# Optimization experiments

Measured on AMD Instinct MI355X. Metric: run time of the kernel, lower is better.

The kernel has to match this reference:

```python
import jax, jax.numpy as jnp
import numpy as np
import math

B, S, H = 4, 2048, 1024
EMBED_DIM = 1024


def setup_inputs() -> dict:
    key = jax.random.key(0)
    ks = jax.random.split(key, 7)
    scale = 1.0 / math.sqrt(H)
    return {
        "xs": jax.random.normal(ks[0], (B, S, H), dtype=jnp.float32),
        "WQ_w": jax.random.normal(ks[1], (EMBED_DIM, H), dtype=jnp.float32) * scale,
        "WQ_b": jax.random.normal(ks[2], (EMBED_DIM,), dtype=jnp.float32) * scale,
        "WK_w": jax.random.normal(ks[3], (EMBED_DIM, H), dtype=jnp.float32) * scale,
        "WK_b": jax.random.normal(ks[4], (EMBED_DIM,), dtype=jnp.float32) * scale,
        "WV_w": jax.random.normal(ks[5], (EMBED_DIM, H), dtype=jnp.float32) * scale,
        "WV_b": jax.random.normal(ks[6], (EMBED_DIM,), dtype=jnp.float32) * scale,
    }


def reference(xs, WQ_w, WQ_b, WK_w, WK_b, WV_w, WV_b):
    # Linear projections (torch nn.Linear: x @ W.T + b)
    q = jnp.einsum('bsh,eh->bse', xs, WQ_w) + WQ_b  # [B,S,E]
    k = jnp.einsum('bsh,eh->bse', xs, WK_w) + WK_b
    v = jnp.einsum('bsh,eh->bse', xs, WV_w) + WV_b
    seq_len = xs.shape[1]
    inv_sqrt_e = 1.0 / math.sqrt(EMBED_DIM)
    qk = jnp.einsum('bqe,bke->bqk', q, k) * inv_sqrt_e  # [B,S,S]
    # causal mask: positions k > q get -inf (triu, diagonal=1)
    causal = jnp.tril(jnp.ones((seq_len, seq_len), dtype=bool))
    qk = jnp.where(causal[None, :, :], qk, -jnp.inf)
    attn = jax.nn.softmax(qk, axis=2)
    y = jnp.einsum('bqk,bke->bqe', attn, v)  # [B,S,E]
    return y
```

## Files before the change

### kernel.cpp

```cpp
#include <hip/hip_runtime.h>
#include <cstdint>
#include <cstddef>

typedef _Float16 f16;
typedef __attribute__((ext_vector_type(4))) _Float16 f16x4;
typedef __attribute__((ext_vector_type(8))) _Float16 f16x8;
typedef __attribute__((ext_vector_type(4))) float f32x4;

static constexpr int BB = 4;
static constexpr int SS = 2048;
static constexpr int EE = 1024;

static constexpr int BM = 128, BN = 128;

__device__ __forceinline__ void gload_lds16(const f16* g, f16* l) {
  __builtin_amdgcn_global_load_lds(
      (const __attribute__((address_space(1))) void*)g,
      (__attribute__((address_space(3))) void*)l, 16, 0, 0);
}

struct Frag {
  int lane, wave, wy, wx, l16, quad, quadx;
  __device__ Frag() {
    const int tid = threadIdx.x;
    lane = tid & 63; wave = tid >> 6;
    wy = wave >> 1; wx = wave & 1;
    l16 = lane & 15; quad = lane >> 4;
    quadx = quad ^ ((l16 >> 2) & 3);
  }
};

struct Stager {
  const f16* g[2];
  int l[2];
  __device__ void init(const f16* base, int ld, const Frag& fr) {
#pragma unroll
    for (int i = 0; i < 2; ++i) {
      const int c = fr.wave * 128 + i * 64 + fr.lane;
      const int row = c >> 2;
      const int kcs = (c & 3) ^ ((c >> 4) & 3);
      g[i] = base + (size_t)row * ld + kcs * 8;
      l[i] = c * 8;
    }
  }
  __device__ __forceinline__ void stage(int ko, f16* lds) const {
    gload_lds16(g[0] + ko, lds + l[0]);
    gload_lds16(g[1] + ko, lds + l[1]);
  }
};

__device__ __forceinline__ void mfma_round(
    const f16* __restrict__ Ash, const f16* __restrict__ Bsh,
    f32x4 acc[4][4], const Frag& fr)
{
  f16x8 af[4], bf[4];
#pragma unroll
  for (int mi = 0; mi < 4; ++mi)
    af[mi] = *(const f16x8*)(Ash + (fr.wy * 64 + mi * 16 + fr.l16) * 32 + fr.quadx * 8);
#pragma unroll
  for (int ni = 0; ni < 4; ++ni)
    bf[ni] = *(const f16x8*)(Bsh + (fr.wx * 64 + ni * 16 + fr.l16) * 32 + fr.quadx * 8);
#pragma unroll
  for (int mi = 0; mi < 4; ++mi)
#pragma unroll
    for (int ni = 0; ni < 4; ++ni)
      acc[mi][ni] = __builtin_amdgcn_mfma_f32_16x16x32_f16(af[mi], bf[ni], acc[mi][ni], 0, 0, 0);
}

__device__ __forceinline__ void gemm_core(
    const f16* __restrict__ A, const f16* __restrict__ Bt,
    int lda, int ldb, int kOuter,
    f16* __restrict__ Ash, f16* __restrict__ Bsh,
    f32x4 acc[4][4], const Frag& fr)
{
  Stager sa, sb;
  sa.init(A, lda, fr);
  sb.init(Bt, ldb, fr);
  for (int kt = 0; kt < kOuter; ++kt) {
    const int ko = kt * 64;
    sa.stage(ko, Ash);       sa.stage(ko + 32, Ash + 128 * 32);
    sb.stage(ko, Bsh);       sb.stage(ko + 32, Bsh + 128 * 32);
    __syncthreads();
    mfma_round(Ash, Bsh, acc, fr);
    mfma_round(Ash + 128 * 32, Bsh + 128 * 32, acc, fr);
    __syncthreads();
  }
}

__device__ __forceinline__ void gemm_core2(
    const f16* __restrict__ A, const f16* __restrict__ Bt,
    int lda, int ldb, int kOuter,
    f16* __restrict__ Ash, f16* __restrict__ Bsh,
    f32x4 acc[4][4], const Frag& fr)
{
  Stager sa, sb;
  sa.init(A, lda, fr);
  sb.init(Bt, ldb, fr);
  sa.stage(0, Ash);  sa.stage(32, Ash + 4096);
  sb.stage(0, Bsh);  sb.stage(32, Bsh + 4096);
  for (int kt = 0; kt < kOuter; ++kt) {
    const int cur = kt & 1, nxt = cur ^ 1;
    if (kt + 1 < kOuter) {
      const int ko = (kt + 1) * 64;
      sa.stage(ko, Ash + nxt * 8192);  sa.stage(ko + 32, Ash + nxt * 8192 + 4096);
      sb.stage(ko, Bsh + nxt * 8192);  sb.stage(ko + 32, Bsh + nxt * 8192 + 4096);
      asm volatile("s_waitcnt vmcnt(8)" ::: "memory");
    } else {
      asm volatile("s_waitcnt vmcnt(0)" ::: "memory");
    }
    __builtin_amdgcn_s_barrier();
    mfma_round(Ash + cur * 8192,        Bsh + cur * 8192,        acc, fr);
    mfma_round(Ash + cur * 8192 + 4096, Bsh + cur * 8192 + 4096, acc, fr);
    __builtin_amdgcn_s_barrier();
  }
}

__global__ __launch_bounds__(256) void cast_all_kernel(
    const float* __restrict__ xs,
    const float* __restrict__ w0, const float* __restrict__ w1, const float* __restrict__ w2,
    f16* __restrict__ Xh, f16* __restrict__ o0, f16* __restrict__ o1, f16* __restrict__ o2)
{
  const int i = blockIdx.x * 256 + threadIdx.x;
  const float* src; f16* dst; int idx;
  if (i < 2097152) {
    src = xs; dst = Xh; idx = i;
  } else {
    const int j = i - 2097152;
    const int w = j >> 18;
    idx = j & 262143;
    src = (w == 0) ? w0 : (w == 1) ? w1 : w2;
    dst = (w == 0) ? o0 : (w == 1) ? o1 : o2;
  }
  const float4 f = ((const float4*)src)[idx];
  f16x4 h;
  h.x = (f16)f.x; h.y = (f16)f.y; h.z = (f16)f.z; h.w = (f16)f.w;
  ((f16x4*)dst)[idx] = h;
}

__global__ __launch_bounds__(256, 2) void proj_kernel(
    const f16* __restrict__ X,
    const f16* __restrict__ Wq, const f16* __restrict__ Wk, const f16* __restrict__ Wv,
    const float* __restrict__ bq, const float* __restrict__ bk, const float* __restrict__ bv,
    f16* __restrict__ Qh, f16* __restrict__ Kh, f16* __restrict__ Vt)
{
  __shared__ __align__(16) f16 smem[3][2][BM * 32];
  Frag fr;
  const int t = blockIdx.x;
  if (t < 512) {
    const int row0 = (t & 63) * BM, col0 = (t >> 6) * BN;
    Stager sa, sw0, sw1;
    sa.init(X + (size_t)row0 * EE, EE, fr);
    sw0.init(Wq + (size_t)col0 * EE, EE, fr);
    sw1.init(Wk + (size_t)col0 * EE, EE, fr);

    f32x4 acc[2][4][4] = {};

    for (int kt = 0; kt < EE / 64; ++kt) {
      const int ko = kt * 64;
      sa.stage(ko, smem[0][0]);   sa.stage(ko + 32, smem[0][1]);
      sw0.stage(ko, smem[1][0]);  sw0.stage(ko + 32, smem[1][1]);
      sw1.stage(ko, smem[2][0]);  sw1.stage(ko + 32, smem[2][1]);
      __syncthreads();
#pragma unroll
      for (int h = 0; h < 2; ++h) {
        f16x8 af[4];
#pragma unroll
        for (int mi = 0; mi < 4; ++mi)
          af[mi] = *(const f16x8*)(smem[0][h] + (fr.wy * 64 + mi * 16 + fr.l16) * 32 + fr.quadx * 8);
#pragma unroll
        for (int z = 0; z < 2; ++z) {
          f16x8 bf[4];
#pragma unroll
          for (int ni = 0; ni < 4; ++ni)
            bf[ni] = *(const f16x8*)(smem[1 + z][h] + (fr.wx * 64 + ni * 16 + fr.l16) * 32 + fr.quadx * 8);
#pragma unroll
          for (int mi = 0; mi < 4; ++mi)
#pragma unroll
            for (int ni = 0; ni < 4; ++ni)
              acc[z][mi][ni] = __builtin_amdgcn_mfma_f32_16x16x32_f16(af[mi], bf[ni], acc[z][mi][ni], 0, 0, 0);
        }
      }
      __syncthreads();
    }

#pragma unroll
    for (int z = 0; z < 2; ++z) {
      const float* bias = (z == 0) ? bq : bk;
      f16* out = (z == 0) ? Qh : Kh;
#pragma unroll
      for (int ni = 0; ni < 4; ++ni) {
        const int c = col0 + fr.wx * 64 + ni * 16 + fr.l16;
        const float bv2 = bias[c];
#pragma unroll
        for (int mi = 0; mi < 4; ++mi) {
          const int r = row0 + fr.wy * 64 + mi * 16 + fr.quad * 4;
#pragma unroll
          for (int i = 0; i < 4; ++i)
            out[(size_t)(r + i) * EE + c] = (f16)(acc[z][mi][ni][i] + bv2);
        }
      }
    }
  } else {
    const int u = t - 512;
    const int row0 = (u & 7) * BM;
    const int sg0 = (u >> 3) * BN;
    const int b = sg0 / SS, s0 = sg0 % SS;
    f32x4 acc[4][4] = {};
    gemm_core(Wv + (size_t)row0 * EE, X + (size_t)sg0 * EE, EE, EE, EE / 64,
              smem[0][0], smem[1][0], acc, fr);
    f16* out = Vt + (size_t)b * EE * SS;
#pragma unroll
    for (int ni = 0; ni < 4; ++ni) {
      const int c = s0 + fr.wx * 64 + ni * 16 + fr.l16;
#pragma unroll
      for (int mi = 0; mi < 4; ++mi) {
        const int r = row0 + fr.wy * 64 + mi * 16 + fr.quad * 4;
#pragma unroll
        for (int i = 0; i < 4; ++i)
          out[(size_t)(r + i) * SS + c] = (f16)(acc[mi][ni][i] + bv[r + i]);
      }
    }
  }
}

__global__ __launch_bounds__(256) void scores_kernel(
    const f16* __restrict__ Q, const f16* __restrict__ Kh, f16* __restrict__ Sc)
{
  __shared__ __align__(16) f16 Ash[2][128 * 64];
  __shared__ __align__(16) f16 Bsh[2][128 * 64];
  const int t = blockIdx.x, b = blockIdx.z;
  int qt = 0;
  while ((qt + 1) * (qt + 2) / 2 <= t) ++qt;
  const int kt = t - qt * (qt + 1) / 2;
  const f16* A  = Q  + (size_t)b * SS * EE + (size_t)qt * BM * EE;
  const f16* Bp = Kh + (size_t)b * SS * EE + (size_t)kt * BN * EE;
  f16* out = Sc + (size_t)b * SS * SS;
  Frag fr;
  f32x4 acc[4][4] = {};
  gemm_core2(A, Bp, EE, EE, EE / 64, Ash[0], Bsh[0], acc, fr);
  const float scale = 0.03125f;
#pragma unroll
  for (int ni = 0; ni < 4; ++ni) {
    const int c = kt * BN + fr.wx * 64 + ni * 16 + fr.l16;
#pragma unroll
    for (int mi = 0; mi < 4; ++mi) {
      const int r = qt * BM + fr.wy * 64 + mi * 16 + fr.quad * 4;
#pragma unroll
      for (int i = 0; i < 4; ++i)
        out[(size_t)(r + i) * SS + c] = (f16)(acc[mi][ni][i] * scale);
    }
  }
}

__global__ __launch_bounds__(256) void softmax_kernel(f16* __restrict__ Sc)
{
  const int q = blockIdx.x, b = blockIdx.y;
  f16* row = Sc + (size_t)b * SS * SS + (size_t)q * SS;
  const int n = q + 1;
  const int kend = ((q >> 7) + 1) << 7;
  const int tid = threadIdx.x;
  const int i0 = tid * 8;

  float v[8];
  if (i0 + 8 <= n) {
    const f16x8 h = *(const f16x8*)(row + i0);
#pragma unroll
    for (int j = 0; j < 8; ++j) v[j] = (float)h[j];
  } else {
#pragma unroll
    for (int j = 0; j < 8; ++j) {
      const int idx = i0 + j;
      v[j] = (idx < n) ? (float)row[idx] : -1e30f;
    }
  }

  float m = v[0];
#pragma unroll
  for (int j = 1; j < 8; ++j) m = fmaxf(m, v[j]);
  __shared__ float red[4];
#pragma unroll
  for (int off = 32; off > 0; off >>= 1) m = fmaxf(m, __shfl_down(m, off));
  if ((tid & 63) == 0) red[tid >> 6] = m;
  __syncthreads();
  m = fmaxf(fmaxf(red[0], red[1]), fmaxf(red[2], red[3]));

  float sum = 0.f;
#pragma unroll
  for (int j = 0; j < 8; ++j) {
    v[j] = (i0 + j < n) ? __expf(v[j] - m) : 0.f;
    sum += v[j];
  }
#pragma unroll
  for (int off = 32; off > 0; off >>= 1) sum += __shfl_down(sum, off);
  __syncthreads();
  if ((tid & 63) == 0) red[tid >> 6] = sum;
  __syncthreads();
  sum = red[0] + red[1] + red[2] + red[3];
  const float inv = 1.f / sum;

  if (i0 < kend) {
    f16x8 h;
#pragma unroll
    for (int j = 0; j < 8; ++j) h[j] = (f16)(v[j] * inv);
    *(f16x8*)(row + i0) = h;
  }
}

__global__ __launch_bounds__(256) void pv_kernel(
    const f16* __restrict__ P, const f16* __restrict__ Vt, float* __restrict__ Y)
{
  __shared__ __align__(16) f16 Ash[2][128 * 64];
  __shared__ __align__(16) f16 Bsh[2][128 * 64];
  const int t = blockIdx.x;
  const int u = t & 255;
  const int qh = u & 7, et = (u >> 3) & 7, b = u >> 6;
  const int qt = (t < 256) ? (15 - qh) : qh;
  const f16* A  = P  + (size_t)b * SS * SS + (size_t)qt * BM * SS;
  const f16* Bp = Vt + (size_t)b * EE * SS + (size_t)et * BN * SS;
  float* out = Y + (size_t)b * SS * EE;
  Frag fr;
  f32x4 acc[4][4] = {};
  gemm_core2(A, Bp, SS, SS, (qt + 1) * 2, Ash[0], Bsh[0], acc, fr);
#pragma unroll
  for (int ni = 0; ni < 4; ++ni) {
    const int c = et * BN + fr.wx * 64 + ni * 16 + fr.l16;
#pragma unroll
    for (int mi = 0; mi < 4; ++mi) {
      const int r = qt * BM + fr.wy * 64 + mi * 16 + fr.quad * 4;
#pragma unroll
      for (int i = 0; i < 4; ++i)
        out[(size_t)(r + i) * EE + c] = acc[mi][ni][i];
    }
  }
}

extern "C" void kernel_launch(void* const* d_in, const int* in_sizes, int n_in,
                              void* d_out, int out_size, void* d_ws, size_t ws_size,
                              hipStream_t stream)
{
  const float* xs  = (const float*)d_in[0];
  const float* WQw = (const float*)d_in[1];
  const float* WQb = (const float*)d_in[2];
  const float* WKw = (const float*)d_in[3];
  const float* WKb = (const float*)d_in[4];
  const float* WVw = (const float*)d_in[5];
  const float* WVb = (const float*)d_in[6];

  const size_t ME = (size_t)BB * SS * EE;
  const size_t WE = (size_t)EE * EE;

  f16* Xh = (f16*)d_ws;
  f16* Wq = Xh + ME;
  f16* Wk = Wq + WE;
  f16* Wv = Wk + WE;
  f16* Qh = Wv + WE;
  f16* Kh = Qh + ME;
  f16* Vt = Kh + ME;
  f16* Sc = Vt + ME;

  cast_all_kernel<<<dim3(11264), 256, 0, stream>>>(
      xs, WQw, WKw, WVw, Xh, Wq, Wk, Wv);

  proj_kernel<<<dim3(1024), 256, 0, stream>>>(
      Xh, Wq, Wk, Wv, WQb, WKb, WVb, Qh, Kh, Vt);

  const int nTri = (SS / BM) * (SS / BM + 1) / 2;
  scores_kernel<<<dim3(nTri, 1, BB), 256, 0, stream>>>(Qh, Kh, Sc);

  softmax_kernel<<<dim3(SS, BB), 256, 0, stream>>>(Sc);

  pv_kernel<<<dim3(512), 256, 0, stream>>>(Sc, Vt, (float*)d_out);
}
```

Before: 261.0 us.

## Fuse softmax into scores epilogue with deferred row-sum normalization in PV

After: 269.1 us. +3.1%, slower.

```diff
diff --git a/kernel.cpp b/kernel.cpp
--- a/kernel.cpp
+++ b/kernel.cpp
@@ -118,9 +118,11 @@
 __global__ __launch_bounds__(256) void cast_all_kernel(
     const float* __restrict__ xs,
     const float* __restrict__ w0, const float* __restrict__ w1, const float* __restrict__ w2,
-    f16* __restrict__ Xh, f16* __restrict__ o0, f16* __restrict__ o1, f16* __restrict__ o2)
+    f16* __restrict__ Xh, f16* __restrict__ o0, f16* __restrict__ o1, f16* __restrict__ o2,
+    float* __restrict__ rowsum)
 {
   const int i = blockIdx.x * 256 + threadIdx.x;
+  if (i < BB * SS) rowsum[i] = 0.f;
   const float* src; f16* dst; int idx;
   if (i < 2097152) {
     src = xs; dst = Xh; idx = i;
@@ -224,10 +226,12 @@
 }
 
 __global__ __launch_bounds__(256) void scores_kernel(
-    const f16* __restrict__ Q, const f16* __restrict__ Kh, f16* __restrict__ Sc)
+    const f16* __restrict__ Q, const f16* __restrict__ Kh, f16* __restrict__ Sc,
+    float* __restrict__ rowsum)
 {
   __shared__ __align__(16) f16 Ash[2][128 * 64];
   __shared__ __align__(16) f16 Bsh[2][128 * 64];
+  __shared__ float rpart[128][16];
   const int t = blockIdx.x, b = blockIdx.z;
   int qt = 0;
   while ((qt + 1) * (qt + 2) / 2 <= t) ++qt;
@@ -238,7 +242,13 @@
   Frag fr;
   f32x4 acc[4][4] = {};
   gemm_core2(A, Bp, EE, EE, EE / 64, Ash[0], Bsh[0], acc, fr);
+
+  const int tid = threadIdx.x;
+  for (int z = tid; z < 128 * 16; z += 256) ((float*)rpart)[z] = 0.f;
+
   const float scale = 0.03125f;
+  const bool diag = (qt == kt);
+  float part[4][4] = {};
 #pragma unroll
   for (int ni = 0; ni < 4; ++ni) {
     const int c = kt * BN + fr.wx * 64 + ni * 16 + fr.l16;
@@ -246,68 +256,34 @@
     for (int mi = 0; mi < 4; ++mi) {
       const int r = qt * BM + fr.wy * 64 + mi * 16 + fr.quad * 4;
 #pragma unroll
-      for (int i = 0; i < 4; ++i)
-        out[(size_t)(r + i) * SS + c] = (f16)(acc[mi][ni][i] * scale);
-    }
-  }
-}
-
-__global__ __launch_bounds__(256) void softmax_kernel(f16* __restrict__ Sc)
-{
-  const int q = blockIdx.x, b = blockIdx.y;
-  f16* row = Sc + (size_t)b * SS * SS + (size_t)q * SS;
-  const int n = q + 1;
-  const int kend = ((q >> 7) + 1) << 7;
-  const int tid = threadIdx.x;
-  const int i0 = tid * 8;
-
-  float v[8];
-  if (i0 + 8 <= n) {
-    const f16x8 h = *(const f16x8*)(row + i0);
-#pragma unroll
-    for (int j = 0; j < 8; ++j) v[j] = (float)h[j];
-  } else {
-#pragma unroll
-    for (int j = 0; j < 8; ++j) {
-      const int idx = i0 + j;
-      v[j] = (idx < n) ? (float)row[idx] : -1e30f;
-    }
-  }
-
-  float m = v[0];
-#pragma unroll
-  for (int j = 1; j < 8; ++j) m = fmaxf(m, v[j]);
-  __shared__ float red[4];
-#pragma unroll
-  for (int off = 32; off > 0; off >>= 1) m = fmaxf(m, __shfl_down(m, off));
-  if ((tid & 63) == 0) red[tid >> 6] = m;
+      for (int i = 0; i < 4; ++i) {
+        float e = __expf(acc[mi][ni][i] * scale);
+        if (diag && c > r + i) e = 0.f;
+        out[(size_t)(r + i) * SS + c] = (f16)e;
+        part[mi][i] += e;
+      }
+    }
+  }
   __syncthreads();
-  m = fmaxf(fmaxf(red[0], red[1]), fmaxf(red[2], red[3]));
-
-  float sum = 0.f;
-#pragma unroll
-  for (int j = 0; j < 8; ++j) {
-    v[j] = (i0 + j < n) ? __expf(v[j] - m) : 0.f;
-    sum += v[j];
-  }
-#pragma unroll
-  for (int off = 32; off > 0; off >>= 1) sum += __shfl_down(sum, off);
+#pragma unroll
+  for (int mi = 0; mi < 4; ++mi)
+#pragma unroll
+    for (int i = 0; i < 4; ++i) {
+      const int lr = fr.wy * 64 + mi * 16 + fr.quad * 4 + i;
+      atomicAdd(&rpart[lr][fr.l16], part[mi][i]);
+    }
   __syncthreads();
-  if ((tid & 63) == 0) red[tid >> 6] = sum;
-  __syncthreads();
-  sum = red[0] + red[1] + red[2] + red[3];
-  const float inv = 1.f / sum;
-
-  if (i0 < kend) {
-    f16x8 h;
-#pragma unroll
-    for (int j = 0; j < 8; ++j) h[j] = (f16)(v[j] * inv);
-    *(f16x8*)(row + i0) = h;
+  if (tid < 128) {
+    float s = 0.f;
+#pragma unroll
+    for (int j = 0; j < 16; ++j) s += rpart[tid][j];
+    atomicAdd(&rowsum[(size_t)b * SS + qt * BM + tid], s);
   }
 }
 
 __global__ __launch_bounds__(256) void pv_kernel(
-    const f16* __restrict__ P, const f16* __restrict__ Vt, float* __restrict__ Y)
+    const f16* __restrict__ P, const f16* __restrict__ Vt,
+    const float* __restrict__ rowsum, float* __restrict__ Y)
 {
   __shared__ __align__(16) f16 Ash[2][128 * 64];
   __shared__ __align__(16) f16 Bsh[2][128 * 64];
@@ -321,6 +297,13 @@
   Frag fr;
   f32x4 acc[4][4] = {};
   gemm_core2(A, Bp, SS, SS, (qt + 1) * 2, Ash[0], Bsh[0], acc, fr);
+  float invr[4][4];
+#pragma unroll
+  for (int mi = 0; mi < 4; ++mi)
+#pragma unroll
+    for (int i = 0; i < 4; ++i)
+      invr[mi][i] = 1.0f /
+          rowsum[(size_t)b * SS + qt * BM + fr.wy * 64 + mi * 16 + fr.quad * 4 + i];
 #pragma unroll
   for (int ni = 0; ni < 4; ++ni) {
     const int c = et * BN + fr.wx * 64 + ni * 16 + fr.l16;
@@ -329,7 +312,7 @@
       const int r = qt * BM + fr.wy * 64 + mi * 16 + fr.quad * 4;
 #pragma unroll
       for (int i = 0; i < 4; ++i)
-        out[(size_t)(r + i) * EE + c] = acc[mi][ni][i];
+        out[(size_t)(r + i) * EE + c] = acc[mi][ni][i] * invr[mi][i];
     }
   }
 }
@@ -357,17 +340,16 @@
   f16* Kh = Qh + ME;
   f16* Vt = Kh + ME;
   f16* Sc = Vt + ME;
+  float* Rs = (float*)(Sc + (size_t)BB * SS * SS);
 
   cast_all_kernel<<<dim3(11264), 256, 0, stream>>>(
-      xs, WQw, WKw, WVw, Xh, Wq, Wk, Wv);
+      xs, WQw, WKw, WVw, Xh, Wq, Wk, Wv, Rs);
 
   proj_kernel<<<dim3(1024), 256, 0, stream>>>(
       Xh, Wq, Wk, Wv, WQb, WKb, WVb, Qh, Kh, Vt);
 
   const int nTri = (SS / BM) * (SS / BM + 1) / 2;
-  scores_kernel<<<dim3(nTri, 1, BB), 256, 0, stream>>>(Qh, Kh, Sc);
-
-  softmax_kernel<<<dim3(SS, BB), 256, 0, stream>>>(Sc);
-
-  pv_kernel<<<dim3(512), 256, 0, stream>>>(Sc, Vt, (float*)d_out);
-}
+  scores_kernel<<<dim3(nTri, 1, BB), 256, 0, stream>>>(Qh, Kh, Sc, Rs);
+
+  pv_kernel<<<dim3(512), 256, 0, stream>>>(Sc, Vt, Rs, (float*)d_out);
+}
```
